# Performance work log

Measured on AMD Instinct MI355X. Metric: run time of the kernel, lower is better.

## Reference

```python
import jax, jax.numpy as jnp
import numpy as np

B, L, D = 16, 256, 256        # batch, enc positions, enc_out_dim
H, E, V, T = 256, 256, 172, 128  # dec_rnn_h, emb_size, vocab, target_len
INIT = 0.01


def setup_inputs() -> dict:
    key = jax.random.key(0)
    ks = jax.random.split(key, 20)
    u = lambda k, shape, s: jax.random.uniform(k, shape, jnp.float32, -s, s)
    inp = {
        "imgs": jax.random.normal(ks[0], (B, L, D), jnp.float32),
        "target_list": jax.random.randint(ks[1], (B, T), 0, V),
        # embedding + LSTMCell (torch layout: W_ih [4H, H+E], W_hh [4H, H])
        "emb": jax.random.normal(ks[2], (V, E), jnp.float32) * 0.02,
        "W_ih": u(ks[3], (4 * H, H + E), 1.0 / np.sqrt(H)),
        "W_hh": u(ks[4], (4 * H, H), 1.0 / np.sqrt(H)),
        "b_ih": u(ks[5], (4 * H,), 1.0 / np.sqrt(H)),
        "b_hh": u(ks[6], (4 * H,), 1.0 / np.sqrt(H)),
        # attention / output projections (no bias)
        "W1": u(ks[7], (D, D), 1.0 / np.sqrt(D)),
        "W2": u(ks[8], (D, H), 1.0 / np.sqrt(H)),
        "W3": u(ks[9], (H, H + D), 1.0 / np.sqrt(H + D)),
        "Wout": u(ks[10], (V, H), 1.0 / np.sqrt(H)),
        "beta": u(ks[11], (D,), INIT),
        # init decoder linears (with bias)
        "wh_W": u(ks[12], (H, D), 1.0 / np.sqrt(D)),
        "wh_b": u(ks[13], (H,), 1.0 / np.sqrt(D)),
        "wc_W": u(ks[14], (H, D), 1.0 / np.sqrt(D)),
        "wc_b": u(ks[15], (H,), 1.0 / np.sqrt(D)),
        "wo_W": u(ks[16], (H, D), 1.0 / np.sqrt(D)),
        "wo_b": u(ks[17], (H,), 1.0 / np.sqrt(D)),
    }
    return inp


def _forward(imgs, emb, W_ih, W_hh, b_ih, b_hh, W1, W2, W3, Wout, beta,
             wh_W, wh_b, wc_W, wc_b, wo_W, wo_b, target_list):
    # init states from mean-pooled encoder output
    mean_enc = imgs.mean(axis=1)                       # [B, D]
    h = jnp.tanh(mean_enc @ wh_W.T + wh_b)             # [B, H]
    c = jnp.tanh(mean_enc @ wc_W.T + wc_b)
    o = jnp.tanh(mean_enc @ wo_W.T + wo_b)

    enc_proj = jnp.einsum('bld,ed->ble', imgs, W1)     # W_1(enc_out), step-invariant

    def step(carry, tgt_t):
        h, c, o = carry
        prev_y = emb[tgt_t]                            # [B, E]
        inp = jnp.concatenate([prev_y, o], axis=1)     # [B, E+H]
        gates = inp @ W_ih.T + b_ih + h @ W_hh.T + b_hh  # [B, 4H]
        i_g, f_g, g_g, o_g = jnp.split(gates, 4, axis=1)
        c_new = jax.nn.sigmoid(f_g) * c + jax.nn.sigmoid(i_g) * jnp.tanh(g_g)
        h_new = jax.nn.sigmoid(o_g) * jnp.tanh(c_new)
        # Bahdanau attention
        alpha = jnp.tanh(enc_proj + (h_new @ W2.T)[:, None, :])   # [B, L, D]
        score = jnp.einsum('bld,d->bl', alpha, beta)
        attn = jax.nn.softmax(score, axis=-1)                     # [B, L]
        ctx = jnp.einsum('bl,bld->bd', attn, imgs)                # [B, D]
        o_new = jnp.tanh(jnp.concatenate([h_new, ctx], axis=1) @ W3.T)  # [B, H]
        logit = jax.nn.softmax(o_new @ Wout.T, axis=1)            # [B, V]
        return (h_new, c_new, o_new), logit

    _, logits = jax.lax.scan(step, (h, c, o), target_list.T)      # [T, B, V]
    return jnp.transpose(logits, (1, 0, 2))                       # [B, T, V]


def reference(imgs, target_list, emb, W_ih, W_hh, b_ih, b_hh, W1, W2, W3,
              Wout, beta, wh_W, wh_b, wc_W, wc_b, wo_W, wo_b):
    return _forward(imgs, emb, W_ih, W_hh, b_ih, b_hh, W1, W2, W3, Wout, beta,
                    wh_W, wh_b, wc_W, wc_b, wo_W, wo_b, target_list)
```

## Files before the change

kernel.cpp:

```cpp
#include <hip/hip_runtime.h>

typedef unsigned int u32;


#define OFF_BAR   0ull
#define OFF_PSE   16384ull
#define OFF_STH   65536ull
#define OFF_PQH   98304ull
#define OFF_PCTX  622592ull
#define OFF_OALL  1146880ull
#define OFF_GTOK  3244032ull

__device__ __forceinline__ float sigm(float x){ return 1.0f/(1.0f+__expf(-x)); }
__device__ __forceinline__ float tanh_f(float x){ return 1.0f - 2.0f/(1.0f+__expf(2.0f*x)); }

__device__ __forceinline__ float blo(u32 q){ u32 x = q<<16; float f; __builtin_memcpy(&f,&x,4); return f; }
__device__ __forceinline__ float bhi(u32 q){ u32 x = q & 0xffff0000u; float f; __builtin_memcpy(&f,&x,4); return f; }
__device__ __forceinline__ u32 f2bu(float f){ u32 x; __builtin_memcpy(&x,&f,4); x = x + 0x7fffu + ((x>>16)&1u); return x>>16; }

struct F8 { float v[8]; };
__device__ __forceinline__ F8 ld8f(const float* q){
  F8 r; float4 a = *(const float4*)q; float4 b = *(const float4*)(q+4);
  r.v[0]=a.x;r.v[1]=a.y;r.v[2]=a.z;r.v[3]=a.w;r.v[4]=b.x;r.v[5]=b.y;r.v[6]=b.z;r.v[7]=b.w;
  return r;
}
__device__ __forceinline__ float dot8(const F8& w, const float* x){
  float4 a = *(const float4*)x; float4 b = *(const float4*)(x+4);
  return w.v[0]*a.x + w.v[1]*a.y + w.v[2]*a.z + w.v[3]*a.w
       + w.v[4]*b.x + w.v[5]*b.y + w.v[6]*b.z + w.v[7]*b.w;
}
__device__ __forceinline__ float dot8r(const float* wr, const float* x){
  float4 a = *(const float4*)x; float4 b = *(const float4*)(x+4);
  return wr[0]*a.x + wr[1]*a.y + wr[2]*a.z + wr[3]*a.w
       + wr[4]*b.x + wr[5]*b.y + wr[6]*b.z + wr[7]*b.w;
}

__device__ __forceinline__ float cohload(const float* p){
  u32 x = __hip_atomic_load((const u32*)p, __ATOMIC_RELAXED, __HIP_MEMORY_SCOPE_AGENT);
  float f; __builtin_memcpy(&f,&x,4); return f;
}
__device__ __forceinline__ void cohstore(float* p, float v){
  u32 x; __builtin_memcpy(&x,&v,4);
  __hip_atomic_store((u32*)p, x, __ATOMIC_RELAXED, __HIP_MEMORY_SCOPE_AGENT);
}

__device__ __forceinline__ void wait_flags(u32* gf, u32 seq){
  if (threadIdx.x < 16){
    while (__hip_atomic_load(gf + threadIdx.x*16, __ATOMIC_RELAXED, __HIP_MEMORY_SCOPE_AGENT) < seq){
      __builtin_amdgcn_s_sleep(1);
    }
  }
  __syncthreads();
}
__device__ __forceinline__ void publish_flag(u32* myf, u32 seq){
  __hip_atomic_store(myf, seq, __ATOMIC_RELEASE, __HIP_MEMORY_SCOPE_AGENT);
}
__device__ __forceinline__ void publish_flag_fast(u32* myf, u32 seq){
  asm volatile("s_waitcnt vmcnt(0)" ::: "memory");
  __hip_atomic_store(myf, seq, __ATOMIC_RELAXED, __HIP_MEMORY_SCOPE_AGENT);
}

extern "C" __global__ __launch_bounds__(256)
void k_init(char* __restrict__ ws){
  u32* bar = (u32*)(ws + OFF_BAR);
  const int gt = blockIdx.x*256 + threadIdx.x;
  if (gt < 4096) bar[gt] = 0u;
}

extern "C" __global__ __launch_bounds__(256, 1)
void k_main(const float* __restrict__ imgs, const int* __restrict__ tgt,
            const float* __restrict__ emb,  const float* __restrict__ W_ih,
            const float* __restrict__ W_hh, const float* __restrict__ b_ih,
            const float* __restrict__ b_hh, const float* __restrict__ W1,
            const float* __restrict__ W2,   const float* __restrict__ W3,
            const float* __restrict__ beta, const float* __restrict__ whW,
            const float* __restrict__ whb,  const float* __restrict__ wcW,
            const float* __restrict__ wcb,  const float* __restrict__ woW,
            const float* __restrict__ wob,  char* __restrict__ ws)
{
  const int tid = threadIdx.x, bid = blockIdx.x;
  const int g = bid & 15, w = bid >> 4, u0 = w*16;

  u32*   gf   = (u32*)(ws + OFF_BAR) + g*256;
  u32*   myf  = gf + w*16;
  float* stH  = (float*)(ws + OFF_STH);
  float* pQH  = (float*)(ws + OFF_PQH);
  float* pCTX = (float*)(ws + OFF_PCTX);
  float* pSE  = (float*)(ws + OFF_PSE);
  float* oAll = (float*)(ws + OFF_OALL);
  float* gtok = (float*)(ws + OFF_GTOK);

  __shared__ __align__(16) float sImg[16*256];
  __shared__ __align__(16) float sEnc[16*256];
  __shared__ __align__(16) float sPimg[16*256];
  __shared__ __align__(16) float sPool[768];
  __shared__ __align__(16) float sHprev[256];
  __shared__ __align__(16) float sO[256];
  __shared__ __align__(16) float sHw2[256];
  __shared__ float sBeta[256];
  __shared__ float sG[64];
  __shared__ float sHown[16];
  __shared__ float sC[16];
  __shared__ float sE[16];
  __shared__ float sE2[16];

  sBeta[tid] = beta[tid];

  for (int r=0; r<3; r++){
    const int tk = bid + 256*r;
    __syncthreads();
    if (tk < 688){
      const int v = tk>>2, q = tk&3;
      sPool[512 + tid] = emb[(size_t)v*256 + tid];
      __syncthreads();
      const int j = q*256 + tid;
      const float* wr = W_ih + (size_t)j*512;
      float a = 0.f;
      #pragma unroll 8
      for (int c=0; c<32; c++) a += dot8(ld8f(wr + c*8), sPool + 512 + c*8);
      gtok[(size_t)v*1024 + j] = a + b_ih[j] + b_hh[j];
    } else {
      __syncthreads();
    }
  }
  __syncthreads();

  { const size_t r0 = (size_t)(g*256 + w*16);
    for (int ri=0; ri<16; ri++) sImg[ri*256+tid] = imgs[(r0+ri)*256 + tid];
    __syncthreads();
    { float acc[16];
      #pragma unroll
      for (int ri=0; ri<16; ri++) acc[ri]=0.f;
      const float* w1r = W1 + (size_t)tid*256;
      for (int c=0; c<32; c++){
        F8 wv = ld8f(w1r + c*8);
        #pragma unroll
        for (int ri=0; ri<16; ri++) acc[ri] += dot8(wv, sImg + ri*256 + c*8);
      }
      for (int ri=0; ri<16; ri++) sEnc[ri*256+tid] = acc[ri];
    }
    { float acc[16];
      #pragma unroll
      for (int ri=0; ri<16; ri++) acc[ri]=0.f;
      const float* w3cr = W3 + (size_t)tid*512 + 256;
      for (int c=0; c<32; c++){
        F8 wv = ld8f(w3cr + c*8);
        #pragma unroll
        for (int ri=0; ri<16; ri++) acc[ri] += dot8(wv, sImg + ri*256 + c*8);
      }
      for (int ri=0; ri<16; ri++) sPimg[ri*256+tid] = acc[ri];
    }
  }
  __syncthreads();

  { float m = 0.f;
    for (int l=0; l<256; l++) m += imgs[((size_t)g*256 + l)*256 + tid];
    sPool[tid] = m * (1.0f/256.0f);
  }
  __syncthreads();
  { const float* whr = whW + (size_t)tid*256;
    const float* wor = woW + (size_t)tid*256;
    float ah=0.f, ao=0.f;
    for (int c=0; c<32; c++){
      ah += dot8(ld8f(whr + c*8), sPool + c*8);
      ao += dot8(ld8f(wor + c*8), sPool + c*8);
    }
    sHprev[tid] = tanhf(ah + whb[tid]);
    sO[tid]     = tanhf(ao + wob[tid]);
  }
  { const int j = tid>>4, sub = tid&15, u = u0 + j;
    float ac=0.f;
    #pragma unroll
    for (int c=0; c<2; c++)
      ac += dot8(ld8f(wcW + (size_t)u*256 + sub*16 + c*8), sPool + sub*16 + c*8);
    ac += __shfl_xor(ac,1); ac += __shfl_xor(ac,2); ac += __shfl_xor(ac,4); ac += __shfl_xor(ac,8);
    if (sub == 0) sC[j] = tanhf(ac + wcb[u]);
  }

  const int rl = tid>>2, p = tid&3;
  const int unit = rl & 15, gate = rl >> 4;
  const int grow = gate*256 + u0 + unit;
  float wior[64], whhr[64];
  { const float* wio = W_ih + (size_t)grow*512 + 256 + p*64;
    const float* whh = W_hh + (size_t)grow*256 +       p*64;
    #pragma unroll
    for (int c=0; c<8; c++){
      F8 a = ld8f(wio + c*8);
      F8 b = ld8f(whh + c*8);
      #pragma unroll
      for (int i=0; i<8; i++){ wior[c*8+i] = a.v[i]; whhr[c*8+i] = b.v[i]; }
    }
  }
  u32 w2p[128];
  { const float* w2r = W2 + (size_t)tid*256;
    #pragma unroll
    for (int c=0; c<128; c++)
      w2p[c] = f2bu(w2r[2*c]) | (f2bu(w2r[2*c+1]) << 16);
  }
  float w3h[16];
  { F8 a = ld8f(W3 + (size_t)tid*512 + u0);
    F8 b = ld8f(W3 + (size_t)tid*512 + u0 + 8);
    #pragma unroll
    for (int i=0; i<8; i++){ w3h[i] = a.v[i]; w3h[8+i] = b.v[i]; }
  }
  const int* tgt_g = tgt + g*128;
  const float* gtok_row = gtok + grow;

  __syncthreads();
  if (tid == 0) publish_flag(myf, 1u);
  wait_flags(gf, 1u);

  for (int t=0; t<128; t++){
    const int par = t & 1;
    const int y = tgt_g[t];
    const float gyv = gtok_row[(size_t)y*1024];

    { float acc = 0.f;
      const float* xo = sO     + p*64;
      const float* xh = sHprev + p*64;
      #pragma unroll
      for (int c=0; c<8; c++){
        acc += dot8r(wior + c*8, xo + c*8);
        acc += dot8r(whhr + c*8, xh + c*8);
      }
      acc += __shfl_xor(acc, 1); acc += __shfl_xor(acc, 2);
      if (p == 0) sG[rl] = acc + gyv;
    }
    __syncthreads();
    if (tid < 16){
      float ig = sG[tid], fg = sG[16+tid], gg = sG[32+tid], og = sG[48+tid];
      float cn = sigm(fg)*sC[tid] + sigm(ig)*tanh_f(gg);
      float hn = sigm(og)*tanh_f(cn);
      sC[tid] = cn;
      sHown[tid] = hn;
      cohstore(stH + par*4096 + g*256 + u0 + tid, hn);
      if (tid == 0) publish_flag_fast(myf, 2u*t + 2u);
    }
    __syncthreads();
    { float qh = 0.f;
      #pragma unroll
      for (int k=0; k<16; k++) qh += w3h[k] * sHown[k];
      cohstore(pQH + ((size_t)(par*16 + g)*16 + w)*256 + tid, qh);
    }

    wait_flags(gf, 2u*t + 2u);
    sHprev[tid] = cohload(stH + par*4096 + g*256 + tid);
    __syncthreads();
    { float a = 0.f;
      #pragma unroll
      for (int c=0; c<128; c++){
        u32 q = w2p[c];
        a += blo(q)*sHprev[2*c] + bhi(q)*sHprev[2*c+1];
      }
      sHw2[tid] = a;
    }
    __syncthreads();
    { const int li = tid>>4, sub = tid&15;
      const float* ep = sEnc + li*256;
      float sc = 0.f;
      #pragma unroll
      for (int i=0; i<16; i++){ int d = i*16 + sub; sc += tanh_f(ep[d] + sHw2[d]) * sBeta[d]; }
      sc += __shfl_xor(sc,1); sc += __shfl_xor(sc,2); sc += __shfl_xor(sc,4); sc += __shfl_xor(sc,8);
      if (sub == 0) sE[li] = __expf(sc);
    }
    __syncthreads();
    { float pv = 0.f;
      #pragma unroll
      for (int li2=0; li2<16; li2++) pv += sE[li2] * sPimg[li2*256 + tid];
      cohstore(pCTX + ((size_t)(par*16 + g)*16 + w)*256 + tid, pv);
    }
    if (tid == 0){
      float se = 0.f;
      #pragma unroll
      for (int j=0; j<16; j++) se += sE[j];
      cohstore(pSE + (par*16 + g)*16 + w, se);
    }
    __syncthreads();
    if (tid == 0) publish_flag_fast(myf, 2u*t + 3u);

    wait_flags(gf, 2u*t + 3u);
    if (tid < 16) sE2[tid] = cohload(pSE + (par*16 + g)*16 + tid);
    float qh = 0.f, pv = 0.f;
    { const float* qb = pQH  + (size_t)(par*16 + g)*4096 + tid;
      const float* cb = pCTX + (size_t)(par*16 + g)*4096 + tid;
      #pragma unroll
      for (int j=0; j<16; j++){ qh += cohload(qb + j*256); pv += cohload(cb + j*256); }
    }
    __syncthreads();
    { float se = 0.f;
      #pragma unroll
      for (int j=0; j<16; j++) se += sE2[j];
      float o = tanh_f(qh + pv/se);
      sO[tid] = o;
      if ((tid>>4) == w) oAll[((size_t)t*16 + g)*256 + tid] = o;
    }
    __syncthreads();
  }
}

extern "C" __global__ __launch_bounds__(256)
void k_logits(const float* __restrict__ Wout, char* __restrict__ ws, float* __restrict__ out){
  __shared__ __align__(16) float sO_[256];
  __shared__ __align__(16) float sRed[256];
  const int tid = threadIdx.x, bid = blockIdx.x;
  const float* oAll = (const float*)(ws + OFF_OALL);
  for (int r=0; r<8; r++){
    const int q = bid*8 + r;
    const int b = q >> 7, t = q & 127;
    __syncthreads();
    sO_[tid] = oAll[((size_t)t*16 + b)*256 + tid];
    __syncthreads();
    float lg = 0.f;
    if (tid < 172){
      const float* wr = Wout + (size_t)tid*256;
      #pragma unroll 8
      for (int c=0; c<32; c++) lg += dot8(ld8f(wr + c*8), sO_ + c*8);
    }
    sRed[tid] = (tid < 172) ? lg : -1e30f;
    __syncthreads();
    for (int s2=128; s2>0; s2>>=1){ if (tid < s2) sRed[tid] = fmaxf(sRed[tid], sRed[tid+s2]); __syncthreads(); }
    const float mx = sRed[0];
    __syncthreads();
    const float ev = (tid < 172) ? __expf(lg - mx) : 0.f;
    sRed[tid] = ev;
    __syncthreads();
    for (int s2=128; s2>0; s2>>=1){ if (tid < s2) sRed[tid] += sRed[tid+s2]; __syncthreads(); }
    const float inv = 1.0f / sRed[0];
    if (tid < 172) out[((size_t)b*128 + t)*172 + tid] = ev * inv;
    __syncthreads();
  }
}

extern "C" void kernel_launch(void* const* d_in, const int* in_sizes, int n_in,
                              void* d_out, int out_size, void* d_ws, size_t ws_size,
                              hipStream_t stream) {
  (void)in_sizes; (void)n_in; (void)out_size; (void)ws_size;
  char* ws = (char*)d_ws;
  k_init<<<16, 256, 0, stream>>>(ws);
  k_main<<<256, 256, 0, stream>>>(
      (const float*)d_in[0],  (const int*)d_in[1],  (const float*)d_in[2],
      (const float*)d_in[3],  (const float*)d_in[4], (const float*)d_in[5],
      (const float*)d_in[6],  (const float*)d_in[7], (const float*)d_in[8],
      (const float*)d_in[9],  (const float*)d_in[11], (const float*)d_in[12],
      (const float*)d_in[13], (const float*)d_in[14], (const float*)d_in[15],
      (const float*)d_in[16], (const float*)d_in[17], ws);
  k_logits<<<256, 256, 0, stream>>>((const float*)d_in[10], ws, (float*)d_out);
}
```

Baseline: 1.438 ms.

## Replace flag barriers with tagged 64-bit value-plus-step words in persistent LSTM decoder

Each cross-block value (h, query partials, context partials, softmax sums) is now stored together with a step tag in a single 64-bit relaxed atomic. Consumers spin on the tag itself instead of waiting on separate per-block flags, which removes the two flag-publish/wait rounds per step and the vmcnt drains they needed. The W_hh·h partial for the next step is also computed early, off the gate critical path. In exchange each store and load moves twice the bytes and polls per element, and the double-buffer parity is dropped for some buffers, which leans on tags to keep steps from overlapping.

```diff
diff --git a/kernel.cpp b/kernel.cpp
--- a/kernel.cpp
+++ b/kernel.cpp
@@ -1,15 +1,16 @@
 #include <hip/hip_runtime.h>
 
 typedef unsigned int u32;
+typedef unsigned long long u64;
 
 
 #define OFF_BAR   0ull
 #define OFF_PSE   16384ull
-#define OFF_STH   65536ull
-#define OFF_PQH   98304ull
-#define OFF_PCTX  622592ull
-#define OFF_OALL  1146880ull
-#define OFF_GTOK  3244032ull
+#define OFF_STH   32768ull
+#define OFF_PQH   65536ull
+#define OFF_PCTX  1114112ull
+#define OFF_OALL  1638400ull
+#define OFF_GTOK  3735552ull
 
 __device__ __forceinline__ float sigm(float x){ return 1.0f/(1.0f+__expf(-x)); }
 __device__ __forceinline__ float tanh_f(float x){ return 1.0f - 2.0f/(1.0f+__expf(2.0f*x)); }
@@ -35,14 +36,17 @@
        + wr[4]*b.x + wr[5]*b.y + wr[6]*b.z + wr[7]*b.w;
 }
 
-__device__ __forceinline__ float cohload(const float* p){
-  u32 x = __hip_atomic_load((const u32*)p, __ATOMIC_RELAXED, __HIP_MEMORY_SCOPE_AGENT);
-  float f; __builtin_memcpy(&f,&x,4); return f;
-}
-__device__ __forceinline__ void cohstore(float* p, float v){
-  u32 x; __builtin_memcpy(&x,&v,4);
-  __hip_atomic_store((u32*)p, x, __ATOMIC_RELAXED, __HIP_MEMORY_SCOPE_AGENT);
-}
+__device__ __forceinline__ u64 cohload64(const u64* p){
+  return __hip_atomic_load(p, __ATOMIC_RELAXED, __HIP_MEMORY_SCOPE_AGENT);
+}
+__device__ __forceinline__ void cohstore64(u64* p, u64 v){
+  __hip_atomic_store(p, v, __ATOMIC_RELAXED, __HIP_MEMORY_SCOPE_AGENT);
+}
+__device__ __forceinline__ u64 packtv(float v, u32 tag){
+  u32 b; __builtin_memcpy(&b,&v,4); return (u64)b | ((u64)tag<<32);
+}
+__device__ __forceinline__ float unpv(u64 x){ u32 b=(u32)x; float f; __builtin_memcpy(&f,&b,4); return f; }
+__device__ __forceinline__ u32 untag(u64 x){ return (u32)(x>>32); }
 
 __device__ __forceinline__ void wait_flags(u32* gf, u32 seq){
   if (threadIdx.x < 16){
@@ -54,10 +58,6 @@
 }
 __device__ __forceinline__ void publish_flag(u32* myf, u32 seq){
   __hip_atomic_store(myf, seq, __ATOMIC_RELEASE, __HIP_MEMORY_SCOPE_AGENT);
-}
-__device__ __forceinline__ void publish_flag_fast(u32* myf, u32 seq){
-  asm volatile("s_waitcnt vmcnt(0)" ::: "memory");
-  __hip_atomic_store(myf, seq, __ATOMIC_RELAXED, __HIP_MEMORY_SCOPE_AGENT);
 }
 
 extern "C" __global__ __launch_bounds__(256)
@@ -81,12 +81,12 @@
   const int tid = threadIdx.x, bid = blockIdx.x;
   const int g = bid & 15, w = bid >> 4, u0 = w*16;
 
-  u32*   gf   = (u32*)(ws + OFF_BAR) + g*256;
-  u32*   myf  = gf + w*16;
-  float* stH  = (float*)(ws + OFF_STH);
-  float* pQH  = (float*)(ws + OFF_PQH);
-  float* pCTX = (float*)(ws + OFF_PCTX);
-  float* pSE  = (float*)(ws + OFF_PSE);
+  u32* gf   = (u32*)(ws + OFF_BAR) + g*256;
+  u32* myf  = gf + w*16;
+  u64* stH  = (u64*)(ws + OFF_STH);
+  u64* pQH  = (u64*)(ws + OFF_PQH);
+  u64* pCTX = (u64*)(ws + OFF_PCTX);
+  u64* pSE  = (u64*)(ws + OFF_PSE);
   float* oAll = (float*)(ws + OFF_OALL);
   float* gtok = (float*)(ws + OFF_GTOK);
 
@@ -210,19 +210,22 @@
   if (tid == 0) publish_flag(myf, 1u);
   wait_flags(gf, 1u);
 
+  float hpart = 0.f;
+  { const float* xh = sHprev + p*64;
+    #pragma unroll
+    for (int c=0; c<8; c++) hpart += dot8r(whhr + c*8, xh + c*8);
+  }
+
   for (int t=0; t<128; t++){
     const int par = t & 1;
+    const u32 tag = (u32)t + 1u;
     const int y = tgt_g[t];
     const float gyv = gtok_row[(size_t)y*1024];
 
-    { float acc = 0.f;
-      const float* xo = sO     + p*64;
-      const float* xh = sHprev + p*64;
-      #pragma unroll
-      for (int c=0; c<8; c++){
-        acc += dot8r(wior + c*8, xo + c*8);
-        acc += dot8r(whhr + c*8, xh + c*8);
-      }
+    { float acc = hpart;
+      const float* xo = sO + p*64;
+      #pragma unroll
+      for (int c=0; c<8; c++) acc += dot8r(wior + c*8, xo + c*8);
       acc += __shfl_xor(acc, 1); acc += __shfl_xor(acc, 2);
       if (p == 0) sG[rl] = acc + gyv;
     }
@@ -233,18 +236,20 @@
       float hn = sigm(og)*tanh_f(cn);
       sC[tid] = cn;
       sHown[tid] = hn;
-      cohstore(stH + par*4096 + g*256 + u0 + tid, hn);
-      if (tid == 0) publish_flag_fast(myf, 2u*t + 2u);
+      cohstore64(stH + g*256 + u0 + tid, packtv(hn, tag));
     }
     __syncthreads();
     { float qh = 0.f;
       #pragma unroll
       for (int k=0; k<16; k++) qh += w3h[k] * sHown[k];
-      cohstore(pQH + ((size_t)(par*16 + g)*16 + w)*256 + tid, qh);
-    }
-
-    wait_flags(gf, 2u*t + 2u);
-    sHprev[tid] = cohload(stH + par*4096 + g*256 + tid);
+      cohstore64(pQH + ((size_t)(par*16 + g)*16 + w)*256 + tid, packtv(qh, tag));
+    }
+
+    { const u64* hp = stH + g*256 + tid;
+      u64 x;
+      do { x = cohload64(hp); } while (untag(x) != tag);
+      sHprev[tid] = unpv(x);
+    }
     __syncthreads();
     { float a = 0.f;
       #pragma unroll
@@ -267,30 +272,61 @@
     { float pv = 0.f;
       #pragma unroll
       for (int li2=0; li2<16; li2++) pv += sE[li2] * sPimg[li2*256 + tid];
-      cohstore(pCTX + ((size_t)(par*16 + g)*16 + w)*256 + tid, pv);
+      cohstore64(pCTX + ((size_t)g*16 + w)*256 + tid, packtv(pv, tag));
     }
     if (tid == 0){
       float se = 0.f;
       #pragma unroll
       for (int j=0; j<16; j++) se += sE[j];
-      cohstore(pSE + (par*16 + g)*16 + w, se);
-    }
-    __syncthreads();
-    if (tid == 0) publish_flag_fast(myf, 2u*t + 3u);
-
-    wait_flags(gf, 2u*t + 3u);
-    if (tid < 16) sE2[tid] = cohload(pSE + (par*16 + g)*16 + tid);
-    float qh = 0.f, pv = 0.f;
-    { const float* qb = pQH  + (size_t)(par*16 + g)*4096 + tid;
-      const float* cb = pCTX + (size_t)(par*16 + g)*4096 + tid;
-      #pragma unroll
-      for (int j=0; j<16; j++){ qh += cohload(qb + j*256); pv += cohload(cb + j*256); }
+      cohstore64(pSE + g*16 + w, packtv(se, tag));
+    }
+    { float hp2 = 0.f;
+      const float* xh = sHprev + p*64;
+      #pragma unroll
+      for (int c=0; c<8; c++) hp2 += dot8r(whhr + c*8, xh + c*8);
+      hpart = hp2;
+    }
+
+    if (tid < 16){
+      u64 x;
+      const u64* sp = pSE + g*16 + tid;
+      do { x = cohload64(sp); } while (untag(x) != tag);
+      sE2[tid] = unpv(x);
+    }
+    float qh = 0.f, pvs = 0.f;
+    { const u64* qb = pQH + (size_t)(par*16 + g)*4096 + tid;
+      u64 v[16];
+      for (;;){
+        #pragma unroll
+        for (int j=0; j<16; j++) v[j] = cohload64(qb + j*256);
+        u32 ok = 1;
+        #pragma unroll
+        for (int j=0; j<16; j++) ok &= (untag(v[j]) == tag) ? 1u : 0u;
+        if (ok) break;
+        __builtin_amdgcn_s_sleep(1);
+      }
+      #pragma unroll
+      for (int j=0; j<16; j++) qh += unpv(v[j]);
+    }
+    { const u64* cb = pCTX + (size_t)g*4096 + tid;
+      u64 v[16];
+      for (;;){
+        #pragma unroll
+        for (int j=0; j<16; j++) v[j] = cohload64(cb + j*256);
+        u32 ok = 1;
+        #pragma unroll
+        for (int j=0; j<16; j++) ok &= (untag(v[j]) == tag) ? 1u : 0u;
+        if (ok) break;
+        __builtin_amdgcn_s_sleep(1);
+      }
+      #pragma unroll
+      for (int j=0; j<16; j++) pvs += unpv(v[j]);
     }
     __syncthreads();
     { float se = 0.f;
       #pragma unroll
       for (int j=0; j<16; j++) se += sE2[j];
-      float o = tanh_f(qh + pv/se);
+      float o = tanh_f(qh + pvs/se);
       sO[tid] = o;
       if ((tid>>4) == w) oAll[((size_t)t*16 + g)*256 + tid] = o;
     }
```

Result: slower. 1.655 ms (+15.1%).
